# Performance work log

Hardware: AMD Instinct MI355X
Metric: run time of the kernel (lower is better)

## Reference

```python
import jax, jax.numpy as jnp
import numpy as np

P = 4   # patch_size
H = 8   # num_heads


def setup_inputs() -> dict:
    key = jax.random.key(0)
    k0, k1, k2 = jax.random.split(key, 3)
    B, C, R = 8, 8, 64
    E = C * P ** 3  # 512
    s = 1.0 / np.sqrt(E)
    x = jax.random.normal(k0, (B, C, R, R, R), jnp.float32)
    in_proj_w = jax.random.normal(k1, (3 * E, E), jnp.float32) * s
    in_proj_b = jnp.zeros((3 * E,), jnp.float32)
    out_proj_w = jax.random.normal(k2, (E, E), jnp.float32) * s
    out_proj_b = jnp.zeros((E,), jnp.float32)
    return {"x": x, "in_proj_w": in_proj_w, "in_proj_b": in_proj_b,
            "out_proj_w": out_proj_w, "out_proj_b": out_proj_b}


def reference(x, in_proj_w, in_proj_b, out_proj_w, out_proj_b):
    B, C, Rx, Ry, Rz = x.shape
    p = P
    nx, ny, nz = Rx // p, Ry // p, Rz // p
    N = nx * ny * nz
    E = C * p ** 3
    dh = E // H

    # cyclic shift: move last patch to front == roll by +p on each spatial axis
    x = jnp.roll(x, (p, p, p), axis=(2, 3, 4))

    # window partition: (B,C,nx,p,ny,p,nz,p) -> (B, N, C*p^3), matching
    # unfold + flatten + permute + flatten of the torch code
    xw = (x.reshape(B, C, nx, p, ny, p, nz, p)
           .transpose(0, 2, 4, 6, 1, 3, 5, 7)
           .reshape(B, N, E))

    # nn.MultiheadAttention with batch_first=False: seq dim = B, batch dim = N
    qkv = jnp.einsum('bne,fe->bnf', xw, in_proj_w) + in_proj_b  # (B, N, 3E)
    q, k, v = jnp.split(qkv, 3, axis=-1)
    q = q.reshape(B, N, H, dh)
    k = k.reshape(B, N, H, dh)
    v = v.reshape(B, N, H, dh)
    scale = 1.0 / np.sqrt(dh)
    # attention over the B (sequence) axis, independently per window n and head h
    att = jax.nn.softmax(jnp.einsum('inhd,jnhd->nhij', q * scale, k), axis=-1)
    o = jnp.einsum('nhij,jnhd->inhd', att, v).reshape(B, N, E)
    o = jnp.einsum('bne,fe->bnf', o, out_proj_w) + out_proj_b  # (B, N, E)

    # torch reassembly via the cat-of-permute loops interleaves windows:
    # out[b, c, px*nx + ix, py*ny + iy, pz*nz + iz] = y[b, ix, iy, iz, c, px, py, pz]
    y = (o.reshape(B, nx, ny, nz, C, p, p, p)
          .transpose(0, 4, 5, 1, 6, 2, 7, 3)
          .reshape(B, C, Rx, Ry, Rz))

    # reverse cyclic shift: roll by -p on each spatial axis
    y = jnp.roll(y, (-p, -p, -p), axis=(2, 3, 4))
    return y
```

## Files before the change

### kernel.cpp

```cpp
#include <hip/hip_runtime.h>

typedef unsigned short u16;
typedef unsigned int u32;
typedef __bf16 bf16x8 __attribute__((ext_vector_type(8)));
typedef float f32x4 __attribute__((ext_vector_type(4)));
typedef unsigned short u16x8 __attribute__((ext_vector_type(8)));

__device__ __forceinline__ u16 f2bf(float f) {
  u32 u = __builtin_bit_cast(u32, f);
  u = (u + 0x7FFFu + ((u >> 16) & 1u)) >> 16;
  return (u16)u;
}
__device__ __forceinline__ float bf2f(u16 h) {
  u32 u = ((u32)h) << 16;
  return __builtin_bit_cast(float, u);
}

#define GLD16(gp, lp) __builtin_amdgcn_global_load_lds( \
    (const __attribute__((address_space(1))) u32*)(const void*)(gp), \
    (__attribute__((address_space(3))) u32*)(void*)(lp), 16, 0, 0)
#define SBAR() __builtin_amdgcn_s_barrier()
#define SCHED0() __builtin_amdgcn_sched_barrier(0)

__global__ __launch_bounds__(256) void cast_both(const float* __restrict__ w_in,
                                                 u16* __restrict__ wq,
                                                 const float* __restrict__ w_out,
                                                 u16* __restrict__ wo) {
  int i = blockIdx.x * 256 + threadIdx.x;
  const float* src = w_in; u16* dst = wq; int idx = i;
  if (i >= 196608) { src = w_out; dst = wo; idx = i - 196608; }
  float4 v = *(const float4*)(src + (size_t)idx * 4);
  ushort4 u;
  u.x = f2bf(v.x); u.y = f2bf(v.y); u.z = f2bf(v.z); u.w = f2bf(v.w);
  *(ushort4*)(dst + (size_t)idx * 4) = u;
}

__global__ __launch_bounds__(256) void permute_in(const float* __restrict__ x,
                                                  u16* __restrict__ xw) {
  __shared__ float lds[128 * 64];
  int t = threadIdx.x;
  int bx = blockIdx.x;
  int b = blockIdx.y;
  int jx = bx >> 4, jy = bx & 15;
#pragma unroll
  for (int it = 0; it < 8; ++it) {
    int idx = t + it * 256;
    int row = idx >> 4, z4 = idx & 15;
    int c = row >> 4, qx = (row >> 2) & 3, qy = row & 3;
    int X = (jx * 4 + qx + 60) & 63;
    int Y = (jy * 4 + qy + 60) & 63;
    float4 v = *(const float4*)(x + ((((size_t)(b * 8 + c) * 64 + X) * 64 + Y) * 64 + z4 * 4));
    *(float4*)(lds + row * 64 + ((z4 ^ (row & 7)) << 2)) = v;
  }
  __syncthreads();
#pragma unroll
  for (int it = 0; it < 8; ++it) {
    int idx = t + it * 256;
    int jz = idx >> 7, r = idx & 127;
    int z4r = (jz + 15) & 15;
    float4 v = *(const float4*)(lds + r * 64 + ((z4r ^ (r & 7)) << 2));
    int nw = jx * 256 + jy * 16 + jz;
    ushort4 u;
    u.x = f2bf(v.x); u.y = f2bf(v.y); u.z = f2bf(v.z); u.w = f2bf(v.w);
    *(ushort4*)(xw + (size_t)(nw * 8 + b) * 512 + r * 4) = u;
  }
}

__global__ __launch_bounds__(512, 1) void gemm_qkv_attn(const u16* __restrict__ A,
                                                        const u16* __restrict__ W,
                                                        const float* __restrict__ bias,
                                                        u16* __restrict__ O) {
  __shared__ u16 smem[57344];
  u16* As = smem;
  u16* Bs = smem + 32768;

  int cpx = gridDim.x >> 3;
  int wg = (blockIdx.x & 7) * cpx + (blockIdx.x >> 3);
  int mb = wg >> 3, h = wg & 7;
  int m0 = mb * 256;

  int tid = threadIdx.x;
  int w = tid >> 6, l = tid & 63;
  int wr = w >> 2, wc = w & 3;
  int lr = l & 15, lg = l >> 4;

  const u16* pa[4]; int dA[4];
#pragma unroll
  for (int i = 0; i < 4; ++i) {
    int slot = w * 256 + i * 64 + l;
    int row = slot >> 3, kg = (slot & 7) ^ (row & 7);
    pa[i] = A + (size_t)(m0 + row) * 512 + kg * 8;
    dA[i] = (w * 256 + i * 64) * 8;
  }
  const u16* pb[3]; int dB[3];
#pragma unroll
  for (int i = 0; i < 3; ++i) {
    int slot = w * 192 + i * 64 + l;
    int row = slot >> 3, kg = (slot & 7) ^ (row & 7);
    int grow = (row >> 6) * 512 + h * 64 + (row & 63);
    pb[i] = W + (size_t)grow * 512 + kg * 8;
    dB[i] = (w * 192 + i * 64) * 8;
  }

  int cx0 = lg ^ (lr & 7), cx1 = cx0 ^ 4;
  int aofs[2] = { (wr * 128 + lr) * 64 + cx0 * 8, (wr * 128 + lr) * 64 + cx1 * 8 };
  int bofs[2] = { (wc * 48 + lr) * 64 + cx0 * 8, (wc * 48 + lr) * 64 + cx1 * 8 };

  f32x4 acc[8][3] = {};

#pragma unroll
  for (int i = 0; i < 4; ++i) GLD16(pa[i], As + dA[i]);
#pragma unroll
  for (int i = 0; i < 3; ++i) GLD16(pb[i], Bs + dB[i]);
  asm volatile("s_waitcnt vmcnt(0)" ::: "memory");
  SCHED0(); SBAR(); SCHED0();

  for (int t = 0; t < 8; ++t) {
    const u16* AsT = As + (t & 1) * 16384;
    const u16* BsT = Bs + (t & 1) * 12288;
    u16* Ad = As + ((t + 1) & 1) * 16384;
    u16* Bd = Bs + ((t + 1) & 1) * 12288;
    int nx = (t + 1) * 64;
    bool st = (t < 7);
    bf16x8 bfr[3][2];
#pragma unroll
    for (int pg = 0; pg < 4; ++pg) {
      bf16x8 afr[2][2];
#pragma unroll
      for (int mi = 0; mi < 2; ++mi)
#pragma unroll
        for (int kk = 0; kk < 2; ++kk)
          afr[mi][kk] = *(const bf16x8*)(AsT + aofs[kk] + (pg * 2 + mi) * 1024);
      if (pg == 0) {
#pragma unroll
        for (int n = 0; n < 3; ++n)
#pragma unroll
          for (int kk = 0; kk < 2; ++kk)
            bfr[n][kk] = *(const bf16x8*)(BsT + bofs[kk] + n * 1024);
      }
      if (pg == 0 && st) { GLD16(pa[0] + nx, Ad + dA[0]); GLD16(pa[1] + nx, Ad + dA[1]); }
      if (pg == 1 && st) { GLD16(pa[2] + nx, Ad + dA[2]); GLD16(pa[3] + nx, Ad + dA[3]); }
      if (pg == 2 && st) { GLD16(pb[0] + nx, Bd + dB[0]); GLD16(pb[1] + nx, Bd + dB[1]); }
      if (pg == 3 && st) { GLD16(pb[2] + nx, Bd + dB[2]); }
      SCHED0();
      __builtin_amdgcn_s_setprio(1);
#pragma unroll
      for (int mi = 0; mi < 2; ++mi)
#pragma unroll
        for (int n = 0; n < 3; ++n)
#pragma unroll
          for (int kk = 0; kk < 2; ++kk)
            acc[pg * 2 + mi][n] =
                __builtin_amdgcn_mfma_f32_16x16x32_bf16(bfr[n][kk], afr[mi][kk],
                                                        acc[pg * 2 + mi][n], 0, 0, 0);
      __builtin_amdgcn_s_setprio(0);
      SCHED0();
    }
    asm volatile("s_waitcnt vmcnt(0)" ::: "memory");
    SCHED0(); SBAR(); SCHED0();
  }

  u16* ct = smem;
#pragma unroll
  for (int n = 0; n < 3; ++n) {
    int col0 = wc * 48 + n * 16 + lg * 4;
    int gcol = ((col0 >> 6) << 9) + (h << 6) + (col0 & 63);
    float4 bv = *(const float4*)(bias + gcol);
#pragma unroll
    for (int m = 0; m < 8; ++m) {
      int row = wr * 128 + m * 16 + lr;
      ushort4 uu;
      uu.x = f2bf(acc[m][n][0] + bv.x);
      uu.y = f2bf(acc[m][n][1] + bv.y);
      uu.z = f2bf(acc[m][n][2] + bv.z);
      uu.w = f2bf(acc[m][n][3] + bv.w);
      *(ushort4*)(ct + row * 200 + col0) = uu;
    }
  }
  __syncthreads();

  int nw2 = tid >> 4, u4 = tid & 15, qi = u4 >> 1, jh = u4 & 1;
  const u16* qrow = ct + (nw2 * 8 + qi) * 200;
  float s4[4];
#pragma unroll
  for (int jj = 0; jj < 4; ++jj) {
    const u16* kr = ct + (nw2 * 8 + jh * 4 + jj) * 200 + 64;
    float sacc = 0.f;
#pragma unroll
    for (int dc = 0; dc < 8; ++dc) {
      u16x8 qv = *(const u16x8*)(qrow + dc * 8);
      u16x8 kv = *(const u16x8*)(kr + dc * 8);
#pragma unroll
      for (int e = 0; e < 8; ++e)
        sacc += bf2f((u16)qv[e]) * bf2f((u16)kv[e]);
    }
    s4[jj] = sacc * 0.125f;
  }
  float r0 = __shfl_xor(s4[0], 1), r1 = __shfl_xor(s4[1], 1);
  float r2 = __shfl_xor(s4[2], 1), r3 = __shfl_xor(s4[3], 1);
  float sm[8];
  if (jh == 0) {
    sm[0] = s4[0]; sm[1] = s4[1]; sm[2] = s4[2]; sm[3] = s4[3];
    sm[4] = r0; sm[5] = r1; sm[6] = r2; sm[7] = r3;
  } else {
    sm[0] = r0; sm[1] = r1; sm[2] = r2; sm[3] = r3;
    sm[4] = s4[0]; sm[5] = s4[1]; sm[6] = s4[2]; sm[7] = s4[3];
  }
  float mx = sm[0];
#pragma unroll
  for (int j = 1; j < 8; ++j) mx = fmaxf(mx, sm[j]);
  float p[8], psum = 0.f;
#pragma unroll
  for (int j = 0; j < 8; ++j) { p[j] = __expf(sm[j] - mx); psum += p[j]; }
  float inv = 1.f / psum;

  float ov[32];
#pragma unroll
  for (int e = 0; e < 32; ++e) ov[e] = 0.f;
#pragma unroll
  for (int j = 0; j < 8; ++j) {
    const u16* vr = ct + (nw2 * 8 + j) * 200 + 128 + jh * 32;
    float pj = p[j] * inv;
#pragma unroll
    for (int dc = 0; dc < 4; ++dc) {
      u16x8 vv = *(const u16x8*)(vr + dc * 8);
#pragma unroll
      for (int e = 0; e < 8; ++e)
        ov[dc * 8 + e] += pj * bf2f((u16)vv[e]);
    }
  }
  u32 pk[16];
#pragma unroll
  for (int e = 0; e < 16; ++e)
    pk[e] = (u32)f2bf(ov[2 * e]) | ((u32)f2bf(ov[2 * e + 1]) << 16);
  u32* dst = (u32*)(O + (size_t)(m0 + nw2 * 8 + qi) * 512 + h * 64 + jh * 32);
#pragma unroll
  for (int q4 = 0; q4 < 4; ++q4) {
    uint4 vq; vq.x = pk[q4 * 4]; vq.y = pk[q4 * 4 + 1];
    vq.z = pk[q4 * 4 + 2]; vq.w = pk[q4 * 4 + 3];
    *(uint4*)(dst + q4 * 4) = vq;
  }
}

__global__ __launch_bounds__(512, 1) void gemm_out_fused(const u16* __restrict__ A,
                                                         const u16* __restrict__ W,
                                                         const float* __restrict__ bias,
                                                         float* __restrict__ outp) {
  __shared__ u16 smem[65536];
  u16* As = smem;
  u16* Bs = smem + 32768;
  float* ldsT = (float*)smem;

  int cpx = gridDim.x >> 3;
  int wg = (blockIdx.x & 7) * cpx + (blockIdx.x >> 3);
  int mb = wg >> 1, nb = wg & 1;
  int m0 = mb * 256, n0 = nb * 256;

  int tid = threadIdx.x;
  int w = tid >> 6, l = tid & 63;
  int wr = w >> 2, wc = w & 3;
  int lr = l & 15, lg = l >> 4;

  const u16* pa[4]; const u16* pb[4]; int dS[4];
#pragma unroll
  for (int i = 0; i < 4; ++i) {
    int slot = w * 256 + i * 64 + l;
    int row = slot >> 3, kg = (slot & 7) ^ (row & 7);
    pa[i] = A + (size_t)(m0 + row) * 512 + kg * 8;
    pb[i] = W + (size_t)(n0 + row) * 512 + kg * 8;
    dS[i] = (w * 256 + i * 64) * 8;
  }

  int cx0 = lg ^ (lr & 7), cx1 = cx0 ^ 4;
  int aofs[2] = { (wr * 128 + lr) * 64 + cx0 * 8, (wr * 128 + lr) * 64 + cx1 * 8 };
  int bofs[2] = { (wc * 64 + lr) * 64 + cx0 * 8, (wc * 64 + lr) * 64 + cx1 * 8 };

  f32x4 acc[8][4] = {};

#pragma unroll
  for (int i = 0; i < 4; ++i) GLD16(pa[i], As + dS[i]);
#pragma unroll
  for (int i = 0; i < 4; ++i) GLD16(pb[i], Bs + dS[i]);
  asm volatile("s_waitcnt vmcnt(0)" ::: "memory");
  SCHED0(); SBAR(); SCHED0();

  for (int t = 0; t < 8; ++t) {
    const u16* AsT = As + (t & 1) * 16384;
    const u16* BsT = Bs + (t & 1) * 16384;
    u16* Ad = As + ((t + 1) & 1) * 16384;
    u16* Bd = Bs + ((t + 1) & 1) * 16384;
    int nx = (t + 1) * 64;
    bool st = (t < 7);
    bf16x8 bfr[4][2];
#pragma unroll
    for (int pg = 0; pg < 4; ++pg) {
      bf16x8 afr[2][2];
#pragma unroll
      for (int mi = 0; mi < 2; ++mi)
#pragma unroll
        for (int kk = 0; kk < 2; ++kk)
          afr[mi][kk] = *(const bf16x8*)(AsT + aofs[kk] + (pg * 2 + mi) * 1024);
      if (pg == 0) {
#pragma unroll
        for (int n = 0; n < 4; ++n)
#pragma unroll
          for (int kk = 0; kk < 2; ++kk)
            bfr[n][kk] = *(const bf16x8*)(BsT + bofs[kk] + n * 1024);
      }
      if (pg == 0 && st) { GLD16(pa[0] + nx, Ad + dS[0]); GLD16(pa[1] + nx, Ad + dS[1]); }
      if (pg == 1 && st) { GLD16(pa[2] + nx, Ad + dS[2]); GLD16(pa[3] + nx, Ad + dS[3]); }
      if (pg == 2 && st) { GLD16(pb[0] + nx, Bd + dS[0]); GLD16(pb[1] + nx, Bd + dS[1]); }
      if (pg == 3 && st) { GLD16(pb[2] + nx, Bd + dS[2]); GLD16(pb[3] + nx, Bd + dS[3]); }
      SCHED0();
      __builtin_amdgcn_s_setprio(1);
#pragma unroll
      for (int mi = 0; mi < 2; ++mi)
#pragma unroll
        for (int n = 0; n < 4; ++n)
#pragma unroll
          for (int kk = 0; kk < 2; ++kk)
            acc[pg * 2 + mi][n] =
                __builtin_amdgcn_mfma_f32_16x16x32_bf16(bfr[n][kk], afr[mi][kk],
                                                        acc[pg * 2 + mi][n], 0, 0, 0);
      __builtin_amdgcn_s_setprio(0);
      SCHED0();
    }
    asm volatile("s_waitcnt vmcnt(0)" ::: "memory");
    SCHED0(); SBAR(); SCHED0();
  }

  __syncthreads();

  float4 bvv[4];
#pragma unroll
  for (int n = 0; n < 4; ++n)
    bvv[n] = *(const float4*)(bias + n0 + wc * 64 + n * 16 + lg * 4);

  int ix = mb >> 3;
  int iy0 = (mb * 2) & 15;
  int jhalf = lr >> 3;

#pragma unroll 1
  for (int b = 0; b < 8; ++b) {
    if ((lr & 7) == b) {
#pragma unroll
      for (int m = 0; m < 8; ++m) {
        int j = wr * 16 + m * 2 + jhalf;
#pragma unroll
        for (int n = 0; n < 4; ++n) {
          int col0 = wc * 64 + n * 16 + lg * 4;
          float4 stv;
          stv.x = acc[m][n][0] + bvv[n].x;
          stv.y = acc[m][n][1] + bvv[n].y;
          stv.z = acc[m][n][2] + bvv[n].z;
          stv.w = acc[m][n][3] + bvv[n].w;
          *(float4*)(ldsT + j * 260 + col0) = stv;
        }
      }
    }
    __syncthreads();
#pragma unroll
    for (int it = 0; it < 4; ++it) {
      int idx = tid + it * 512;
      int w4 = idx & 15, iyr = (idx >> 4) & 1, fl = idx >> 5;
      int cl = fl >> 4, px = (fl >> 2) & 3, py = fl & 3;
      int W0 = (w4 * 4 + 4) & 63;
      int pz = W0 >> 4, iz0 = W0 & 15;
      int fa = fl * 4 + pz;
      int rbase = iyr * 16 + iz0;
      float4 v;
      v.x = ldsT[(rbase + 0) * 260 + fa];
      v.y = ldsT[(rbase + 1) * 260 + fa];
      v.z = ldsT[(rbase + 2) * 260 + fa];
      v.w = ldsT[(rbase + 3) * 260 + fa];
      int c = nb * 4 + cl;
      int uu = (px * 16 + ix + 60) & 63;
      int vv = (py * 16 + iy0 + iyr + 60) & 63;
      *(float4*)(outp + ((((size_t)(b * 8 + c) * 64 + uu) * 64 + vv) * 64 + w4 * 4)) = v;
    }
    __syncthreads();
  }
}

extern "C" void kernel_launch(void* const* d_in, const int* in_sizes, int n_in,
                              void* d_out, int out_size, void* d_ws, size_t ws_size,
                              hipStream_t stream) {
  const float* x     = (const float*)d_in[0];
  const float* w_in  = (const float*)d_in[1];
  const float* b_in  = (const float*)d_in[2];
  const float* w_out = (const float*)d_in[3];
  const float* b_out = (const float*)d_in[4];
  float* out = (float*)d_out;

  char* ws = (char*)d_ws;
  u16* wq  = (u16*)(ws);
  u16* wo  = (u16*)(ws + 1572864);
  u16* xw2 = (u16*)(ws + 2097152);
  u16* o   = (u16*)(ws + 35651584);

  cast_both<<<1024, 256, 0, stream>>>(w_in, wq, w_out, wo);
  permute_in<<<dim3(256, 8), 256, 0, stream>>>(x, xw2);
  gemm_qkv_attn<<<1024, 512, 0, stream>>>(xw2, wq, b_in, o);
  gemm_out_fused<<<256, 512, 0, stream>>>(o, wo, b_out, out);
}
```

Baseline: 132.9 us.

## Keep QKV tile in fp32 LDS and process attention in 32-row chunks

The attention epilogue of the fused QKV GEMM now stages the bias-added accumulators as fp32 in LDS with an XOR swizzle, in 32-row chunks, instead of converting the whole 256-row tile to bf16. Four waves compute scores, softmax (via shuffles) and the PV product per chunk, with one lane per (query, key) pair. This removes the bf16 round-trip on Q/K/V, which improves accuracy, and changes the LDS access pattern. In exchange it adds 16 block barriers and leaves half the waves idle during attention, which may add latency.

```diff
diff --git a/kernel.cpp b/kernel.cpp
--- a/kernel.cpp
+++ b/kernel.cpp
@@ -4,7 +4,6 @@
 typedef unsigned int u32;
 typedef __bf16 bf16x8 __attribute__((ext_vector_type(8)));
 typedef float f32x4 __attribute__((ext_vector_type(4)));
-typedef unsigned short u16x8 __attribute__((ext_vector_type(8)));
 
 __device__ __forceinline__ u16 f2bf(float f) {
   u32 u = __builtin_bit_cast(u32, f);
@@ -73,6 +72,7 @@
   __shared__ u16 smem[57344];
   u16* As = smem;
   u16* Bs = smem + 32768;
+  float* ctf = (float*)smem;
 
   int cpx = gridDim.x >> 3;
   int wg = (blockIdx.x & 7) * cpx + (blockIdx.x >> 3);
@@ -160,85 +160,83 @@
     SCHED0(); SBAR(); SCHED0();
   }
 
-  u16* ct = smem;
+  __syncthreads();
+
+  float4 bvv[3];
 #pragma unroll
   for (int n = 0; n < 3; ++n) {
     int col0 = wc * 48 + n * 16 + lg * 4;
     int gcol = ((col0 >> 6) << 9) + (h << 6) + (col0 & 63);
-    float4 bv = *(const float4*)(bias + gcol);
-#pragma unroll
-    for (int m = 0; m < 8; ++m) {
-      int row = wr * 128 + m * 16 + lr;
-      ushort4 uu;
-      uu.x = f2bf(acc[m][n][0] + bv.x);
-      uu.y = f2bf(acc[m][n][1] + bv.y);
-      uu.z = f2bf(acc[m][n][2] + bv.z);
-      uu.w = f2bf(acc[m][n][3] + bv.w);
-      *(ushort4*)(ct + row * 200 + col0) = uu;
-    }
-  }
-  __syncthreads();
-
-  int nw2 = tid >> 4, u4 = tid & 15, qi = u4 >> 1, jh = u4 & 1;
-  const u16* qrow = ct + (nw2 * 8 + qi) * 200;
-  float s4[4];
-#pragma unroll
-  for (int jj = 0; jj < 4; ++jj) {
-    const u16* kr = ct + (nw2 * 8 + jh * 4 + jj) * 200 + 64;
-    float sacc = 0.f;
-#pragma unroll
-    for (int dc = 0; dc < 8; ++dc) {
-      u16x8 qv = *(const u16x8*)(qrow + dc * 8);
-      u16x8 kv = *(const u16x8*)(kr + dc * 8);
-#pragma unroll
-      for (int e = 0; e < 8; ++e)
-        sacc += bf2f((u16)qv[e]) * bf2f((u16)kv[e]);
-    }
-    s4[jj] = sacc * 0.125f;
-  }
-  float r0 = __shfl_xor(s4[0], 1), r1 = __shfl_xor(s4[1], 1);
-  float r2 = __shfl_xor(s4[2], 1), r3 = __shfl_xor(s4[3], 1);
-  float sm[8];
-  if (jh == 0) {
-    sm[0] = s4[0]; sm[1] = s4[1]; sm[2] = s4[2]; sm[3] = s4[3];
-    sm[4] = r0; sm[5] = r1; sm[6] = r2; sm[7] = r3;
-  } else {
-    sm[0] = r0; sm[1] = r1; sm[2] = r2; sm[3] = r3;
-    sm[4] = s4[0]; sm[5] = s4[1]; sm[6] = s4[2]; sm[7] = s4[3];
-  }
-  float mx = sm[0];
-#pragma unroll
-  for (int j = 1; j < 8; ++j) mx = fmaxf(mx, sm[j]);
-  float p[8], psum = 0.f;
-#pragma unroll
-  for (int j = 0; j < 8; ++j) { p[j] = __expf(sm[j] - mx); psum += p[j]; }
-  float inv = 1.f / psum;
-
-  float ov[32];
-#pragma unroll
-  for (int e = 0; e < 32; ++e) ov[e] = 0.f;
-#pragma unroll
-  for (int j = 0; j < 8; ++j) {
-    const u16* vr = ct + (nw2 * 8 + j) * 200 + 128 + jh * 32;
-    float pj = p[j] * inv;
-#pragma unroll
-    for (int dc = 0; dc < 4; ++dc) {
-      u16x8 vv = *(const u16x8*)(vr + dc * 8);
-#pragma unroll
-      for (int e = 0; e < 8; ++e)
-        ov[dc * 8 + e] += pj * bf2f((u16)vv[e]);
-    }
-  }
-  u32 pk[16];
-#pragma unroll
-  for (int e = 0; e < 16; ++e)
-    pk[e] = (u32)f2bf(ov[2 * e]) | ((u32)f2bf(ov[2 * e + 1]) << 16);
-  u32* dst = (u32*)(O + (size_t)(m0 + nw2 * 8 + qi) * 512 + h * 64 + jh * 32);
-#pragma unroll
-  for (int q4 = 0; q4 < 4; ++q4) {
-    uint4 vq; vq.x = pk[q4 * 4]; vq.y = pk[q4 * 4 + 1];
-    vq.z = pk[q4 * 4 + 2]; vq.w = pk[q4 * 4 + 3];
-    *(uint4*)(dst + q4 * 4) = vq;
+    bvv[n] = *(const float4*)(bias + gcol);
+  }
+
+#pragma unroll
+  for (int c = 0; c < 8; ++c) {
+    if ((c >> 2) == wr) {
+#pragma unroll
+      for (int mm = 0; mm < 2; ++mm) {
+        const int m = (c & 3) * 2 + mm;
+        int row_local = mm * 16 + lr;
+        int skey = ((row_local >> 3) & 3) << 2;
+#pragma unroll
+        for (int n = 0; n < 3; ++n) {
+          int col0 = wc * 48 + n * 16 + lg * 4;
+          float4 stv;
+          stv.x = acc[m][n][0] + bvv[n].x;
+          stv.y = acc[m][n][1] + bvv[n].y;
+          stv.z = acc[m][n][2] + bvv[n].z;
+          stv.w = acc[m][n][3] + bvv[n].w;
+          *(float4*)(ctf + row_local * 204 + (col0 ^ skey)) = stv;
+        }
+      }
+    }
+    __syncthreads();
+    if (w < 4) {
+      int qi = l >> 3, j = l & 7;
+      int K4 = w << 2;
+      const float* qr = ctf + (w * 8 + qi) * 204;
+      const float* kr = ctf + (w * 8 + j) * 204;
+      float sc = 0.f;
+#pragma unroll
+      for (int d = 0; d < 16; ++d) {
+        float4 qv = *(const float4*)(qr + ((d * 4) ^ K4));
+        float4 kv = *(const float4*)(kr + ((64 + d * 4) ^ K4));
+        sc += qv.x * kv.x + qv.y * kv.y + qv.z * kv.z + qv.w * kv.w;
+      }
+      sc *= 0.125f;
+      float mx = sc;
+      mx = fmaxf(mx, __shfl_xor(mx, 1));
+      mx = fmaxf(mx, __shfl_xor(mx, 2));
+      mx = fmaxf(mx, __shfl_xor(mx, 4));
+      float p = __expf(sc - mx);
+      float sum = p;
+      sum += __shfl_xor(sum, 1);
+      sum += __shfl_xor(sum, 2);
+      sum += __shfl_xor(sum, 4);
+      p /= sum;
+      float pr[8];
+      int lb = l & 56;
+#pragma unroll
+      for (int jj = 0; jj < 8; ++jj) pr[jj] = __shfl(p, lb + jj);
+      float ov[8] = {};
+#pragma unroll
+      for (int jj = 0; jj < 8; ++jj) {
+        const float* vr = ctf + (w * 8 + jj) * 204;
+        int b0 = 128 + j * 8;
+        float4 va = *(const float4*)(vr + (b0 ^ K4));
+        float4 vb = *(const float4*)(vr + ((b0 + 4) ^ K4));
+        float pj = pr[jj];
+        ov[0] += pj * va.x; ov[1] += pj * va.y; ov[2] += pj * va.z; ov[3] += pj * va.w;
+        ov[4] += pj * vb.x; ov[5] += pj * vb.y; ov[6] += pj * vb.z; ov[7] += pj * vb.w;
+      }
+      ushort4 r0, r1;
+      r0.x = f2bf(ov[0]); r0.y = f2bf(ov[1]); r0.z = f2bf(ov[2]); r0.w = f2bf(ov[3]);
+      r1.x = f2bf(ov[4]); r1.y = f2bf(ov[5]); r1.z = f2bf(ov[6]); r1.w = f2bf(ov[7]);
+      u16* dst = O + (size_t)(m0 + c * 32 + w * 8 + qi) * 512 + h * 64 + j * 8;
+      *(ushort4*)dst = r0;
+      *(ushort4*)(dst + 4) = r1;
+    }
+    __syncthreads();
   }
 }
 
```

New measurement: 147.3 us. 10.8% more time.
